# Optimization experiments

Measured on AMD Instinct MI355X. Metric: run time of the kernel, lower is better.

Reference implementation:

```python
import jax, jax.numpy as jnp
import numpy as np

EMBED_DIM = 1024
NUM_HEADS = 16
HEAD_DIM = EMBED_DIM // NUM_HEADS


def setup_inputs() -> dict:
    key = jax.random.key(0)
    kx, kq, kk, kv, ko = jax.random.split(key, 5)
    scale = 1.0 / np.sqrt(EMBED_DIM)
    return {
        "x": jax.random.normal(kx, (4, 2048, EMBED_DIM), dtype=jnp.float32),
        # nn.Linear weights are [out, in]; y = x @ W.T
        "w_q": jax.random.normal(kq, (EMBED_DIM, EMBED_DIM), dtype=jnp.float32) * scale,
        "w_k": jax.random.normal(kk, (EMBED_DIM, EMBED_DIM), dtype=jnp.float32) * scale,
        "w_v": jax.random.normal(kv, (EMBED_DIM, EMBED_DIM), dtype=jnp.float32) * scale,
        "w_o": jax.random.normal(ko, (EMBED_DIM, EMBED_DIM), dtype=jnp.float32) * scale,
    }


def reference(x, w_q, w_k, w_v, w_o):
    b, s, _ = x.shape
    # projections (Linear with no bias: x @ W.T)
    q = (x @ w_q.T).reshape(b, s, NUM_HEADS, HEAD_DIM).transpose(0, 2, 1, 3)
    k = (x @ w_k.T).reshape(b, s, NUM_HEADS, HEAD_DIM).transpose(0, 2, 1, 3)
    v = (x @ w_v.T).reshape(b, s, NUM_HEADS, HEAD_DIM).transpose(0, 2, 1, 3)
    # scores: [b, h, s, s]
    scores = jnp.einsum("bhqd,bhkd->bhqk", q, k) / jnp.sqrt(jnp.float32(HEAD_DIM)).astype(x.dtype)
    attn = jax.nn.softmax(scores, axis=-1)
    out = jnp.einsum("bhqk,bhkd->bhqd", attn, v)  # [b, h, s, d]
    out = out.transpose(0, 2, 1, 3).reshape(b, s, EMBED_DIM)
    return out @ w_o.T
```

## Files before the change

### kernel.cpp

```cpp
#include <hip/hip_runtime.h>
#include <math.h>

#define EMBED 1024
#define NHEAD 16
#define HDIM  64
#define BATCH 4
#define SEQ   2048
#define MROWS (BATCH * SEQ)

typedef __attribute__((ext_vector_type(4))) short short4v;
typedef __attribute__((ext_vector_type(8))) short short8;
typedef __attribute__((ext_vector_type(4))) float floatx4;
typedef __attribute__((ext_vector_type(16))) float floatx16;
typedef __attribute__((ext_vector_type(2))) unsigned uint2v;

#if __has_builtin(__builtin_amdgcn_exp2f)
#define EXP2(x) __builtin_amdgcn_exp2f(x)
#else
#define EXP2(x) exp2f(x)
#endif

__device__ __forceinline__ unsigned short f2bf(float f) {
  unsigned u = __float_as_uint(f);
  u += 0x7fffu + ((u >> 16) & 1u);
  return (unsigned short)(u >> 16);
}

#if __has_builtin(__builtin_amdgcn_cvt_pk_bf16_f32)
__device__ __forceinline__ unsigned pack2bf(float lo, float hi) {
  typedef __attribute__((ext_vector_type(2))) __bf16 bf2;
  union { bf2 b; unsigned u; } c;
  c.b = __builtin_amdgcn_cvt_pk_bf16_f32(lo, hi);
  return c.u;
}
#else
__device__ __forceinline__ unsigned pack2bf(float lo, float hi) {
  return ((__float_as_uint(lo) + 0x8000u) >> 16) |
         ((__float_as_uint(hi) + 0x8000u) & 0xffff0000u);
}
#endif

__device__ __forceinline__ uint2v pl32swap(unsigned a, unsigned b) {
#if __has_builtin(__builtin_amdgcn_permlane32_swap)
  return __builtin_amdgcn_permlane32_swap(a, b, false, false);
#else
  uint2v r;
  unsigned ax = (unsigned)__shfl_xor((int)a, 32);
  unsigned bx = (unsigned)__shfl_xor((int)b, 32);
  const int hi = (int)((threadIdx.x & 63) >> 5);
  r[0] = hi ? bx : a;
  r[1] = hi ? b : ax;
  return r;
#endif
}

__device__ __forceinline__ void gl_lds16(const void* g, void* l) {
  __builtin_amdgcn_global_load_lds(
      (const __attribute__((address_space(1))) unsigned int*)g,
      (__attribute__((address_space(3))) unsigned int*)l, 16, 0, 0);
}

__global__ __launch_bounds__(256) void cast_bf16_kernel(
    const float* __restrict__ x,  const float* __restrict__ wq,
    const float* __restrict__ wk, const float* __restrict__ wv,
    const float* __restrict__ wo,
    unsigned short* __restrict__ xb, unsigned short* __restrict__ wb) {
  const size_t NX = (size_t)MROWS * EMBED;
  size_t i4 = ((size_t)blockIdx.x * 256 + threadIdx.x) * 4;
  const float* src;
  unsigned short* dst;
  size_t off;
  if (i4 < NX) {
    src = x; dst = xb; off = i4;
  } else {
    size_t j = i4 - NX;
    int r = (int)(j >> 20);
    off = j & ((1u << 20) - 1);
    src = (r == 0) ? wq : (r == 1) ? wk : (r == 2) ? wv : wo;
    dst = wb + ((size_t)r << 20);
  }
  float4 v = *(const float4*)(src + off);
  ushort4 o;
  o.x = f2bf(v.x); o.y = f2bf(v.y); o.z = f2bf(v.z); o.w = f2bf(v.w);
  *(ushort4*)(dst + off) = o;
}

#define RD_A(bo, mi, ks) (*(const short8*)&LA[(bo) + wr * 8192 + \
    ((mi) * 16 + l15) * 64 + ((((ks) * 4 + quad) ^ (l15 & 7)) * 8)])
#define RD_B(bo, ni, ks) (*(const short8*)&LB[(bo) + hB * 8192 + \
    (rB0 + (ni) * 16 + l15) * 64 + ((((ks) * 4 + quad) ^ (l15 & 7)) * 8)])

__device__ __forceinline__ void gemm_core8(
    const unsigned short* __restrict__ Amat,
    const unsigned short* __restrict__ Bmat,
    int mBase, int nBase,
    unsigned short* LA, unsigned short* LB,
    floatx4 acc[8][4]) {
  const int t = threadIdx.x;
  const int lane = t & 63, wv = t >> 6;
  const int wr = wv >> 2, wc = wv & 3;
  const int quad = lane >> 4, l15 = lane & 15;
  const int hB = wc >> 1, rB0 = (wc & 1) * 64;

  const unsigned short* sA[2][2];
  const unsigned short* sB[2][2];
  unsigned short* dA[2][2];
  unsigned short* dB[2][2];
#pragma unroll
  for (int h = 0; h < 2; ++h)
#pragma unroll
    for (int i = 0; i < 2; ++i) {
      const int c = i * 512 + t;
      const int row = c >> 3, g = (c & 7) ^ (row & 7);
      sA[h][i] = Amat + (size_t)(mBase + h * 128 + row) * EMBED + g * 8;
      sB[h][i] = Bmat + (size_t)(nBase + h * 128 + row) * EMBED + g * 8;
      const int du = h * 8192 + (i * 512 + wv * 64) * 8;
      dA[h][i] = LA + du;
      dB[h][i] = LB + du;
    }

  gl_lds16(sA[0][0], dA[0][0]); gl_lds16(sA[0][1], dA[0][1]);
  gl_lds16(sA[1][0], dA[1][0]); gl_lds16(sA[1][1], dA[1][1]);
  gl_lds16(sB[0][0], dB[0][0]); gl_lds16(sB[0][1], dB[0][1]);
  gl_lds16(sB[1][0], dB[1][0]); gl_lds16(sB[1][1], dB[1][1]);
  gl_lds16(sB[0][0] + 64, dB[0][0] + 16384);
  gl_lds16(sB[0][1] + 64, dB[0][1] + 16384);
  gl_lds16(sB[1][0] + 64, dB[1][0] + 16384);
  gl_lds16(sB[1][1] + 64, dB[1][1] + 16384);

  short8 b[4][2];
  for (int T = 0; T < 16; T += 2) {
#pragma unroll
    for (int hf = 0; hf < 2; ++hf) {
      const int bo = hf * 16384;
#pragma unroll
      for (int p = 0; p < 4; ++p) {
        short8 a[2][2];
        if (p == 0) {
          {
            const int ts = (T + 1 + hf) & 15, tb = (ts & 1) * 16384;
            gl_lds16(sA[0][0] + (size_t)ts * 64, dA[0][0] + tb);
            gl_lds16(sA[0][1] + (size_t)ts * 64, dA[0][1] + tb);
          }
          asm volatile("s_waitcnt vmcnt(6)" ::: "memory");
          __builtin_amdgcn_sched_barrier(0);
          __builtin_amdgcn_s_barrier();
#pragma unroll
          for (int ni = 0; ni < 4; ++ni) {
            b[ni][0] = RD_B(bo, ni, 0);
            b[ni][1] = RD_B(bo, ni, 1);
          }
          a[0][0] = RD_A(bo, 0, 0); a[0][1] = RD_A(bo, 0, 1);
          a[1][0] = RD_A(bo, 1, 0); a[1][1] = RD_A(bo, 1, 1);
        } else {
          const int mi0 = 2 * p;
          a[0][0] = RD_A(bo, mi0, 0);     a[0][1] = RD_A(bo, mi0, 1);
          a[1][0] = RD_A(bo, mi0 + 1, 0); a[1][1] = RD_A(bo, mi0 + 1, 1);
          if (p == 1) {
            const int ts = (T + 1 + hf) & 15, tb = (ts & 1) * 16384;
            gl_lds16(sA[1][0] + (size_t)ts * 64, dA[1][0] + tb);
            gl_lds16(sA[1][1] + (size_t)ts * 64, dA[1][1] + tb);
          } else if (p == 2) {
            const int ts = (T + 2 + hf) & 15, tb = (ts & 1) * 16384;
            gl_lds16(sB[0][0] + (size_t)ts * 64, dB[0][0] + tb);
            gl_lds16(sB[0][1] + (size_t)ts * 64, dB[0][1] + tb);
          } else {
            const int ts = (T + 2 + hf) & 15, tb = (ts & 1) * 16384;
            gl_lds16(sB[1][0] + (size_t)ts * 64, dB[1][0] + tb);
            gl_lds16(sB[1][1] + (size_t)ts * 64, dB[1][1] + tb);
          }
          __builtin_amdgcn_sched_barrier(0);
          __builtin_amdgcn_s_barrier();
        }
        asm volatile("s_waitcnt lgkmcnt(0)" ::: "memory");
        __builtin_amdgcn_sched_barrier(0);
        __builtin_amdgcn_s_setprio(1);
        const int mi0 = 2 * p;
#pragma unroll
        for (int m2 = 0; m2 < 2; ++m2)
#pragma unroll
          for (int ni = 0; ni < 4; ++ni) {
            acc[mi0 + m2][ni] = __builtin_amdgcn_mfma_f32_16x16x32_bf16(
                a[m2][0], b[ni][0], acc[mi0 + m2][ni], 0, 0, 0);
            acc[mi0 + m2][ni] = __builtin_amdgcn_mfma_f32_16x16x32_bf16(
                a[m2][1], b[ni][1], acc[mi0 + m2][ni], 0, 0, 0);
          }
        __builtin_amdgcn_s_setprio(0);
        __builtin_amdgcn_sched_barrier(0);
        __builtin_amdgcn_s_barrier();
      }
    }
  }
  asm volatile("s_waitcnt vmcnt(0)" ::: "memory");
}

__global__ __launch_bounds__(512, 2) void proj_qkv_bf16(
    const unsigned short* __restrict__ xb,
    const unsigned short* __restrict__ wb,
    unsigned short* __restrict__ qkv) {
  const int id = blockIdx.x;
  const int xcd = id & 7;
  const int r = id >> 3;
  const int nIdx = r >> 2;
  const int mBase = (xcd * 4 + (r & 3)) * 256;
  const int nBase = nIdx * 256;

  __shared__ unsigned short LA[32768];
  __shared__ unsigned short LB[32768];

  floatx4 acc[8][4] = {};
  gemm_core8(xb, wb, mBase, nBase, LA, LB, acc);

  const int t = threadIdx.x;
  const int lane = t & 63, wv = t >> 6;
  const int wr = wv >> 2, wc = wv & 3;
  const int quad = lane >> 4, l15 = lane & 15;

  const int which = nBase >> 10;
  const int nloc0 = nBase & 1023;
  unsigned short* out = qkv + (size_t)which * MROWS * EMBED;

  if (which < 2) {
    const float scale = (which == 0) ? 0.18033688f : 1.0f;
#pragma unroll
    for (int mi = 0; mi < 8; ++mi)
#pragma unroll
      for (int ni = 0; ni < 4; ++ni) {
        const int nn = nloc0 + wc * 64 + ni * 16 + l15;
        const int h = nn >> 6, d = nn & 63;
#pragma unroll
        for (int r2 = 0; r2 < 4; ++r2) {
          const int m = mBase + wr * 128 + mi * 16 + quad * 4 + r2;
          const int b = m >> 11, s = m & (SEQ - 1);
          out[(((size_t)(b * NHEAD + h) * SEQ) + s) * HDIM + d] =
              f2bf(acc[mi][ni][r2] * scale);
        }
      }
  } else {
#pragma unroll
    for (int mi = 0; mi < 8; ++mi) {
      const int m0 = mBase + wr * 128 + mi * 16 + quad * 4;
      const int b = m0 >> 11, s0 = m0 & (SEQ - 1);
#pragma unroll
      for (int ni = 0; ni < 4; ++ni) {
        const int nn = nloc0 + wc * 64 + ni * 16 + l15;
        const int h = nn >> 6, d = nn & 63;
        ushort4 pk;
        pk.x = f2bf(acc[mi][ni][0]); pk.y = f2bf(acc[mi][ni][1]);
        pk.z = f2bf(acc[mi][ni][2]); pk.w = f2bf(acc[mi][ni][3]);
        *(ushort4*)&out[((size_t)(b * NHEAD + h) * HDIM + d) * SEQ + s0] = pk;
      }
    }
  }
}

__global__ __launch_bounds__(256, 2) void attn_mfma(
    const unsigned short* __restrict__ qkv,
    unsigned short* __restrict__ aout) {
  const unsigned short* Q = qkv;
  const unsigned short* K = qkv + (size_t)MROWS * EMBED;
  const unsigned short* V = qkv + 2 * (size_t)MROWS * EMBED;

  const int id = blockIdx.x;
  const int xcd = id & 7, slot = id >> 3;
  const int bh = xcd * 8 + (slot >> 3);
  const int qBase = (slot & 7) * 256;

  __shared__ unsigned short Ks[2 * 128 * 64];
  __shared__ unsigned short Vs[2 * 64 * 128];

  const int t = threadIdx.x;
  const int lane = t & 63, w = t >> 6;
  const int h2 = lane >> 5;
  const int q31 = lane & 31;

  const unsigned short* qrowA =
      Q + ((size_t)bh * SEQ + qBase + w * 64 + q31) * HDIM;
  const unsigned short* qrowB = qrowA + 32 * HDIM;
  short8 qaA[4], qaB[4];
#pragma unroll
  for (int ds = 0; ds < 4; ++ds) {
    qaA[ds] = *(const short8*)(qrowA + ds * 16 + h2 * 8);
    qaB[ds] = *(const short8*)(qrowB + ds * 16 + h2 * 8);
  }

  const unsigned short* kbase = K + (size_t)bh * SEQ * HDIM;
  const unsigned short* vbase = V + (size_t)bh * HDIM * SEQ;
  const unsigned short* gk[4];
  const unsigned short* gv[4];
  unsigned short* lk[4];
  unsigned short* lv[4];
#pragma unroll
  for (int i = 0; i < 4; ++i) {
    const int c = i * 256 + t;
    const int krow = c >> 3, kgrp = (c & 7) ^ (krow & 7);
    gk[i] = kbase + (size_t)krow * HDIM + kgrp * 8;
    const int vd = c >> 4, vj = (c & 15) ^ (vd & 15);
    gv[i] = vbase + (size_t)vd * SEQ + vj * 8;
    const int cu = i * 256 + w * 64;
    lk[i] = Ks + cu * 8;
    lv[i] = Vs + cu * 8;
  }

  floatx16 otA0 = {}, otA1 = {};
  floatx16 otB0 = {}, otB1 = {};
  float laccA = 0.0f, laccB = 0.0f;

#pragma unroll
  for (int i = 0; i < 4; ++i) {
    gl_lds16(gk[i], lk[i]);
    gl_lds16(gv[i], lv[i]);
  }

  for (int kt = 0; kt < SEQ; kt += 128) {
    const int cb = (kt >> 7) & 1;
    const int nb = cb ^ 1;
    const int nxt = (kt + 128) & (SEQ - 1);
    const int sOff = nb * 8192;
#pragma unroll
    for (int i = 0; i < 4; ++i) {
      gl_lds16(gk[i] + (size_t)nxt * HDIM, lk[i] + sOff);
      gl_lds16(gv[i] + nxt, lv[i] + sOff);
    }
    __builtin_amdgcn_sched_barrier(0);
    asm volatile("s_waitcnt vmcnt(8)" ::: "memory");
    __builtin_amdgcn_s_barrier();

    const int kOff = cb * 8192;
    const int vOff = cb * 8192;

#pragma unroll
    for (int sub = 0; sub < 2; ++sub) {
      const int koff = sub * 64;

      floatx16 stA0 = {}, stA1 = {}, stB0 = {}, stB1 = {};
      __builtin_amdgcn_s_setprio(1);
#pragma unroll
      for (int ds = 0; ds < 4; ++ds) {
        const int g = ds * 2 + h2;
        const int k0 = koff + q31;
        short8 ka0 = *(const short8*)&Ks[kOff + k0 * 64 + ((g ^ (q31 & 7)) * 8)];
        stA0 = __builtin_amdgcn_mfma_f32_32x32x16_bf16(ka0, qaA[ds], stA0, 0, 0, 0);
        stB0 = __builtin_amdgcn_mfma_f32_32x32x16_bf16(ka0, qaB[ds], stB0, 0, 0, 0);
        const int k1 = koff + 32 + q31;
        short8 ka1 = *(const short8*)&Ks[kOff + k1 * 64 + ((g ^ (q31 & 7)) * 8)];
        stA1 = __builtin_amdgcn_mfma_f32_32x32x16_bf16(ka1, qaA[ds], stA1, 0, 0, 0);
        stB1 = __builtin_amdgcn_mfma_f32_32x32x16_bf16(ka1, qaB[ds], stB1, 0, 0, 0);
      }
      __builtin_amdgcn_s_setprio(0);

      unsigned pkA0[8], pkA1[8], pkB0[8], pkB1[8];
#pragma unroll
      for (int i = 0; i < 8; ++i) {
        float a0 = EXP2(stA0[2 * i]), b0 = EXP2(stA0[2 * i + 1]);
        float a1 = EXP2(stA1[2 * i]), b1 = EXP2(stA1[2 * i + 1]);
        laccA += (a0 + b0) + (a1 + b1);
        pkA0[i] = pack2bf(a0, b0);
        pkA1[i] = pack2bf(a1, b1);
        float c0 = EXP2(stB0[2 * i]), d0 = EXP2(stB0[2 * i + 1]);
        float c1 = EXP2(stB1[2 * i]), d1 = EXP2(stB1[2 * i + 1]);
        laccB += (c0 + d0) + (c1 + d1);
        pkB0[i] = pack2bf(c0, d0);
        pkB1[i] = pack2bf(c1, d1);
      }

      __builtin_amdgcn_s_setprio(1);
#pragma unroll
      for (int sp = 0; sp < 4; ++sp) {
        const unsigned* pA = (sp < 2) ? pkA0 : pkA1;
        const unsigned* pB = (sp < 2) ? pkB0 : pkB1;
        const int off = (sp & 1) * 4;
        uint2v ra0 = pl32swap(pA[off + 0], pA[off + 2]);
        uint2v ra1 = pl32swap(pA[off + 1], pA[off + 3]);
        uint2v rb0 = pl32swap(pB[off + 0], pB[off + 2]);
        uint2v rb1 = pl32swap(pB[off + 1], pB[off + 3]);
        union { unsigned u[4]; short8 v; } pbA, pbB;
        pbA.u[0] = ra0[0]; pbA.u[1] = ra1[0]; pbA.u[2] = ra0[1]; pbA.u[3] = ra1[1];
        pbB.u[0] = rb0[0]; pbB.u[1] = rb1[0]; pbB.u[2] = rb0[1]; pbB.u[3] = rb1[1];

        const int g8 = sub * 8 + sp * 2 + h2;
        const int pos = (g8 ^ (q31 & 15)) * 8;
        short8 va0 = *(const short8*)&Vs[vOff + q31 * 128 + pos];
        otA0 = __builtin_amdgcn_mfma_f32_32x32x16_bf16(va0, pbA.v, otA0, 0, 0, 0);
        otB0 = __builtin_amdgcn_mfma_f32_32x32x16_bf16(va0, pbB.v, otB0, 0, 0, 0);
        short8 va1 = *(const short8*)&Vs[vOff + (32 + q31) * 128 + pos];
        otA1 = __builtin_amdgcn_mfma_f32_32x32x16_bf16(va1, pbA.v, otA1, 0, 0, 0);
        otB1 = __builtin_amdgcn_mfma_f32_32x32x16_bf16(va1, pbB.v, otB1, 0, 0, 0);
      }
      __builtin_amdgcn_s_setprio(0);
    }

    __builtin_amdgcn_sched_barrier(0);
    __builtin_amdgcn_s_barrier();
  }
  asm volatile("s_waitcnt vmcnt(0)" ::: "memory");

  const float totA = laccA + __shfl_xor(laccA, 32);
  const float totB = laccB + __shfl_xor(laccB, 32);
  const float invA = 1.0f / totA;
  const float invB = 1.0f / totB;

  const int b = bh >> 4, hh = bh & 15;
  unsigned short* orowA =
      aout + ((size_t)b * SEQ + qBase + w * 64 + q31) * EMBED + hh * HDIM;
  unsigned short* orowB = orowA + (size_t)32 * EMBED;
#pragma unroll
  for (int rg = 0; rg < 4; ++rg) {
    const int d0 = rg * 8 + h2 * 4;
    ushort4 p0, p1;
    p0.x = f2bf(otA0[4 * rg + 0] * invA); p0.y = f2bf(otA0[4 * rg + 1] * invA);
    p0.z = f2bf(otA0[4 * rg + 2] * invA); p0.w = f2bf(otA0[4 * rg + 3] * invA);
    *(ushort4*)(orowA + d0) = p0;
    p1.x = f2bf(otA1[4 * rg + 0] * invA); p1.y = f2bf(otA1[4 * rg + 1] * invA);
    p1.z = f2bf(otA1[4 * rg + 2] * invA); p1.w = f2bf(otA1[4 * rg + 3] * invA);
    *(ushort4*)(orowA + 32 + d0) = p1;
    ushort4 p2, p3;
    p2.x = f2bf(otB0[4 * rg + 0] * invB); p2.y = f2bf(otB0[4 * rg + 1] * invB);
    p2.z = f2bf(otB0[4 * rg + 2] * invB); p2.w = f2bf(otB0[4 * rg + 3] * invB);
    *(ushort4*)(orowB + d0) = p2;
    p3.x = f2bf(otB1[4 * rg + 0] * invB); p3.y = f2bf(otB1[4 * rg + 1] * invB);
    p3.z = f2bf(otB1[4 * rg + 2] * invB); p3.w = f2bf(otB1[4 * rg + 3] * invB);
    *(ushort4*)(orowB + 32 + d0) = p3;
  }
}

__global__ __launch_bounds__(512, 2) void out_proj_bf16(
    const unsigned short* __restrict__ aout,
    const unsigned short* __restrict__ wb,
    float* __restrict__ Cout) {
  const int id = blockIdx.x;
  const int xcd = id & 7;
  const int r = id >> 3;
  const int nBase = (r >> 2) * 256;
  const int mBase = (xcd * 4 + (r & 3)) * 256;

  __shared__ unsigned short LA[32768];
  __shared__ unsigned short LB[32768];

  floatx4 acc[8][4] = {};
  gemm_core8(aout, wb + ((size_t)3 << 20), mBase, nBase, LA, LB, acc);

  const int t = threadIdx.x;
  const int lane = t & 63, wv = t >> 6;
  const int wr = wv >> 2, wc = wv & 3;
  const int quad = lane >> 4, l15 = lane & 15;

#pragma unroll
  for (int mi = 0; mi < 8; ++mi)
#pragma unroll
    for (int ni = 0; ni < 4; ++ni) {
      const int n = nBase + wc * 64 + ni * 16 + l15;
#pragma unroll
      for (int r2 = 0; r2 < 4; ++r2) {
        const int m = mBase + wr * 128 + mi * 16 + quad * 4 + r2;
        Cout[(size_t)m * EMBED + n] = acc[mi][ni][r2];
      }
    }
}

extern "C" void kernel_launch(void* const* d_in, const int* in_sizes, int n_in,
                              void* d_out, int out_size, void* d_ws, size_t ws_size,
                              hipStream_t stream) {
  const float* x  = (const float*)d_in[0];
  const float* wq = (const float*)d_in[1];
  const float* wk = (const float*)d_in[2];
  const float* wv = (const float*)d_in[3];
  const float* wo = (const float*)d_in[4];
  float* out = (float*)d_out;

  char* ws = (char*)d_ws;
  unsigned short* xb   = (unsigned short*)(ws);
  unsigned short* wb   = (unsigned short*)(ws + (16u << 20));
  unsigned short* qkv  = (unsigned short*)(ws + (26u << 20));
  unsigned short* aout = (unsigned short*)(ws + (76u << 20));

  cast_bf16_kernel<<<12288, 256, 0, stream>>>(x, wq, wk, wv, wo, xb, wb);
  proj_qkv_bf16<<<384, 512, 0, stream>>>(xb, wb, qkv);
  attn_mfma<<<512, 256, 0, stream>>>(qkv, aout);
  out_proj_bf16<<<128, 512, 0, stream>>>(aout, wb, out);
}
```

Baseline: 272.1 us.

## Halve GEMM N-tile to 128 to double block count for projections

Shrinks the projection GEMM tile from 256x256 to 256x128. Each wave now covers 32 columns, the B tile in LDS is halved, and the vmcnt wait depth is adjusted to the fewer loads. The grid grows from 384 to 768 blocks for QKV and from 128 to 256 for the output projection, so more CUs stay busy, especially on out_proj, which previously had only 128 blocks on a 256-CU device. The cost is lower arithmetic intensity per block: A tiles are reloaded twice as often and each LDS read of A feeds half as many MFMAs.

```diff
diff --git a/kernel.cpp b/kernel.cpp
--- a/kernel.cpp
+++ b/kernel.cpp
@@ -87,7 +87,7 @@
 
 #define RD_A(bo, mi, ks) (*(const short8*)&LA[(bo) + wr * 8192 + \
     ((mi) * 16 + l15) * 64 + ((((ks) * 4 + quad) ^ (l15 & 7)) * 8)])
-#define RD_B(bo, ni, ks) (*(const short8*)&LB[(bo) + hB * 8192 + \
+#define RD_B(boB, ni, ks) (*(const short8*)&LB[(boB) + \
     (rB0 + (ni) * 16 + l15) * 64 + ((((ks) * 4 + quad) ^ (l15 & 7)) * 8)])
 
 __device__ __forceinline__ void gemm_core8(
@@ -95,65 +95,60 @@
     const unsigned short* __restrict__ Bmat,
     int mBase, int nBase,
     unsigned short* LA, unsigned short* LB,
-    floatx4 acc[8][4]) {
+    floatx4 acc[8][2]) {
   const int t = threadIdx.x;
   const int lane = t & 63, wv = t >> 6;
   const int wr = wv >> 2, wc = wv & 3;
   const int quad = lane >> 4, l15 = lane & 15;
-  const int hB = wc >> 1, rB0 = (wc & 1) * 64;
+  const int rB0 = wc * 32;
 
   const unsigned short* sA[2][2];
-  const unsigned short* sB[2][2];
+  const unsigned short* sB[2];
   unsigned short* dA[2][2];
-  unsigned short* dB[2][2];
-#pragma unroll
-  for (int h = 0; h < 2; ++h)
-#pragma unroll
-    for (int i = 0; i < 2; ++i) {
-      const int c = i * 512 + t;
-      const int row = c >> 3, g = (c & 7) ^ (row & 7);
-      sA[h][i] = Amat + (size_t)(mBase + h * 128 + row) * EMBED + g * 8;
-      sB[h][i] = Bmat + (size_t)(nBase + h * 128 + row) * EMBED + g * 8;
-      const int du = h * 8192 + (i * 512 + wv * 64) * 8;
-      dA[h][i] = LA + du;
-      dB[h][i] = LB + du;
-    }
+  unsigned short* dB[2];
+#pragma unroll
+  for (int i = 0; i < 2; ++i) {
+    const int c = i * 512 + t;
+    const int row = c >> 3, g = (c & 7) ^ (row & 7);
+    sA[0][i] = Amat + (size_t)(mBase + row) * EMBED + g * 8;
+    sA[1][i] = Amat + (size_t)(mBase + 128 + row) * EMBED + g * 8;
+    sB[i]    = Bmat + (size_t)(nBase + row) * EMBED + g * 8;
+    const int du = (i * 512 + wv * 64) * 8;
+    dA[0][i] = LA + du;
+    dA[1][i] = LA + 8192 + du;
+    dB[i]    = LB + du;
+  }
 
   gl_lds16(sA[0][0], dA[0][0]); gl_lds16(sA[0][1], dA[0][1]);
   gl_lds16(sA[1][0], dA[1][0]); gl_lds16(sA[1][1], dA[1][1]);
-  gl_lds16(sB[0][0], dB[0][0]); gl_lds16(sB[0][1], dB[0][1]);
-  gl_lds16(sB[1][0], dB[1][0]); gl_lds16(sB[1][1], dB[1][1]);
-  gl_lds16(sB[0][0] + 64, dB[0][0] + 16384);
-  gl_lds16(sB[0][1] + 64, dB[0][1] + 16384);
-  gl_lds16(sB[1][0] + 64, dB[1][0] + 16384);
-  gl_lds16(sB[1][1] + 64, dB[1][1] + 16384);
-
-  short8 b[4][2];
+  gl_lds16(sB[0], dB[0]);       gl_lds16(sB[1], dB[1]);
+  gl_lds16(sB[0] + 64, dB[0] + 8192);
+  gl_lds16(sB[1] + 64, dB[1] + 8192);
+
+  short8 b[2][2];
   for (int T = 0; T < 16; T += 2) {
 #pragma unroll
     for (int hf = 0; hf < 2; ++hf) {
       const int bo = hf * 16384;
+      const int boB = hf * 8192;
 #pragma unroll
       for (int p = 0; p < 4; ++p) {
         short8 a[2][2];
+        const int mi0 = 2 * p;
         if (p == 0) {
           {
             const int ts = (T + 1 + hf) & 15, tb = (ts & 1) * 16384;
             gl_lds16(sA[0][0] + (size_t)ts * 64, dA[0][0] + tb);
             gl_lds16(sA[0][1] + (size_t)ts * 64, dA[0][1] + tb);
           }
-          asm volatile("s_waitcnt vmcnt(6)" ::: "memory");
+          asm volatile("s_waitcnt vmcnt(4)" ::: "memory");
           __builtin_amdgcn_sched_barrier(0);
           __builtin_amdgcn_s_barrier();
-#pragma unroll
-          for (int ni = 0; ni < 4; ++ni) {
-            b[ni][0] = RD_B(bo, ni, 0);
-            b[ni][1] = RD_B(bo, ni, 1);
-          }
+          b[0][0] = RD_B(boB, 0, 0); b[0][1] = RD_B(boB, 0, 1);
+          b[1][0] = RD_B(boB, 1, 0); b[1][1] = RD_B(boB, 1, 1);
           a[0][0] = RD_A(bo, 0, 0); a[0][1] = RD_A(bo, 0, 1);
           a[1][0] = RD_A(bo, 1, 0); a[1][1] = RD_A(bo, 1, 1);
         } else {
-          const int mi0 = 2 * p;
           a[0][0] = RD_A(bo, mi0, 0);     a[0][1] = RD_A(bo, mi0, 1);
           a[1][0] = RD_A(bo, mi0 + 1, 0); a[1][1] = RD_A(bo, mi0 + 1, 1);
           if (p == 1) {
@@ -161,13 +156,9 @@
             gl_lds16(sA[1][0] + (size_t)ts * 64, dA[1][0] + tb);
             gl_lds16(sA[1][1] + (size_t)ts * 64, dA[1][1] + tb);
           } else if (p == 2) {
-            const int ts = (T + 2 + hf) & 15, tb = (ts & 1) * 16384;
-            gl_lds16(sB[0][0] + (size_t)ts * 64, dB[0][0] + tb);
-            gl_lds16(sB[0][1] + (size_t)ts * 64, dB[0][1] + tb);
-          } else {
-            const int ts = (T + 2 + hf) & 15, tb = (ts & 1) * 16384;
-            gl_lds16(sB[1][0] + (size_t)ts * 64, dB[1][0] + tb);
-            gl_lds16(sB[1][1] + (size_t)ts * 64, dB[1][1] + tb);
+            const int ts = (T + 2 + hf) & 15, tbB = (ts & 1) * 8192;
+            gl_lds16(sB[0] + (size_t)ts * 64, dB[0] + tbB);
+            gl_lds16(sB[1] + (size_t)ts * 64, dB[1] + tbB);
           }
           __builtin_amdgcn_sched_barrier(0);
           __builtin_amdgcn_s_barrier();
@@ -175,11 +166,10 @@
         asm volatile("s_waitcnt lgkmcnt(0)" ::: "memory");
         __builtin_amdgcn_sched_barrier(0);
         __builtin_amdgcn_s_setprio(1);
-        const int mi0 = 2 * p;
 #pragma unroll
         for (int m2 = 0; m2 < 2; ++m2)
 #pragma unroll
-          for (int ni = 0; ni < 4; ++ni) {
+          for (int ni = 0; ni < 2; ++ni) {
             acc[mi0 + m2][ni] = __builtin_amdgcn_mfma_f32_16x16x32_bf16(
                 a[m2][0], b[ni][0], acc[mi0 + m2][ni], 0, 0, 0);
             acc[mi0 + m2][ni] = __builtin_amdgcn_mfma_f32_16x16x32_bf16(
@@ -203,12 +193,12 @@
   const int r = id >> 3;
   const int nIdx = r >> 2;
   const int mBase = (xcd * 4 + (r & 3)) * 256;
-  const int nBase = nIdx * 256;
+  const int nBase = nIdx * 128;
 
   __shared__ unsigned short LA[32768];
-  __shared__ unsigned short LB[32768];
-
-  floatx4 acc[8][4] = {};
+  __shared__ unsigned short LB[16384];
+
+  floatx4 acc[8][2] = {};
   gemm_core8(xb, wb, mBase, nBase, LA, LB, acc);
 
   const int t = threadIdx.x;
@@ -225,8 +215,8 @@
 #pragma unroll
     for (int mi = 0; mi < 8; ++mi)
 #pragma unroll
-      for (int ni = 0; ni < 4; ++ni) {
-        const int nn = nloc0 + wc * 64 + ni * 16 + l15;
+      for (int ni = 0; ni < 2; ++ni) {
+        const int nn = nloc0 + wc * 32 + ni * 16 + l15;
         const int h = nn >> 6, d = nn & 63;
 #pragma unroll
         for (int r2 = 0; r2 < 4; ++r2) {
@@ -242,8 +232,8 @@
       const int m0 = mBase + wr * 128 + mi * 16 + quad * 4;
       const int b = m0 >> 11, s0 = m0 & (SEQ - 1);
 #pragma unroll
-      for (int ni = 0; ni < 4; ++ni) {
-        const int nn = nloc0 + wc * 64 + ni * 16 + l15;
+      for (int ni = 0; ni < 2; ++ni) {
+        const int nn = nloc0 + wc * 32 + ni * 16 + l15;
         const int h = nn >> 6, d = nn & 63;
         ushort4 pk;
         pk.x = f2bf(acc[mi][ni][0]); pk.y = f2bf(acc[mi][ni][1]);
@@ -431,13 +421,13 @@
   const int id = blockIdx.x;
   const int xcd = id & 7;
   const int r = id >> 3;
-  const int nBase = (r >> 2) * 256;
+  const int nBase = (r >> 2) * 128;
   const int mBase = (xcd * 4 + (r & 3)) * 256;
 
   __shared__ unsigned short LA[32768];
-  __shared__ unsigned short LB[32768];
-
-  floatx4 acc[8][4] = {};
+  __shared__ unsigned short LB[16384];
+
+  floatx4 acc[8][2] = {};
   gemm_core8(aout, wb + ((size_t)3 << 20), mBase, nBase, LA, LB, acc);
 
   const int t = threadIdx.x;
@@ -448,8 +438,8 @@
 #pragma unroll
   for (int mi = 0; mi < 8; ++mi)
 #pragma unroll
-    for (int ni = 0; ni < 4; ++ni) {
-      const int n = nBase + wc * 64 + ni * 16 + l15;
+    for (int ni = 0; ni < 2; ++ni) {
+      const int n = nBase + wc * 32 + ni * 16 + l15;
 #pragma unroll
       for (int r2 = 0; r2 < 4; ++r2) {
         const int m = mBase + wr * 128 + mi * 16 + quad * 4 + r2;
@@ -475,7 +465,7 @@
   unsigned short* aout = (unsigned short*)(ws + (76u << 20));
 
   cast_bf16_kernel<<<12288, 256, 0, stream>>>(x, wq, wk, wv, wo, xb, wb);
-  proj_qkv_bf16<<<384, 512, 0, stream>>>(xb, wb, qkv);
+  proj_qkv_bf16<<<768, 512, 0, stream>>>(xb, wb, qkv);
   attn_mfma<<<512, 256, 0, stream>>>(qkv, aout);
-  out_proj_bf16<<<128, 512, 0, stream>>>(aout, wb, out);
-}
+  out_proj_bf16<<<256, 512, 0, stream>>>(aout, wb, out);
+}
```

Result: faster. 265.7 us (-2.4%).
